# Optimization experiments

Measured on AMD Instinct MI355X. Metric: run time of the kernel, lower is better.

## Reference

```python
import jax, jax.numpy as jnp
import numpy as np

DAYS, TOPICS, T, E, H, DH = 30, 20, 128, 300, 256, 64

def _lstm_layer(x, Wih, Whh, b):
    # x: [B, T, D] -> (outputs [B, T, H], final hidden [B, H]); torch gate order i,f,g,o
    B = x.shape[0]
    Hh = Whh.shape[1]
    def step(carry, xt):
        h, c = carry
        g = xt @ Wih.T + h @ Whh.T + b
        i, f, gg, o = jnp.split(g, 4, axis=-1)
        c = jax.nn.sigmoid(f) * c + jax.nn.sigmoid(i) * jnp.tanh(gg)
        h = jax.nn.sigmoid(o) * jnp.tanh(c)
        return (h, c), h
    init = (jnp.zeros((B, Hh), x.dtype), jnp.zeros((B, Hh), x.dtype))
    (hT, _), ys = jax.lax.scan(step, init, jnp.swapaxes(x, 0, 1))
    return jnp.swapaxes(ys, 0, 1), hT

def _lstm2(x, W0, U0, b0, W1, U1, b1):
    # 2-layer LSTM (eval mode, dropout inactive). Returns layer-1 outputs and
    # LAYER-0 final hidden (the torch code indexes final_hidden_state[0]).
    y0, h0T = _lstm_layer(x, W0, U0, b0)
    y1, _ = _lstm_layer(y0, W1, U1, b1)
    return y1, h0T

def _attn_topic(out, final, w1_W, w1_b):
    # out [topics, H], final [H]; keep sorted weights until cumulative sum exceeds 0.8 (inclusive)
    score = (out @ w1_W.T + w1_b) @ final            # [topics]
    attn = jax.nn.softmax(score, axis=0)
    order = jnp.argsort(-attn)
    s = attn[order]
    keep = (jnp.cumsum(s) - s) <= 0.8                # exclusive-cumsum <= 0.8 == torch break-inclusive
    return jnp.sum((s * keep)[:, None] * out[order], axis=0)

def _forward(X, previous_labels,
             txt_Wih0, txt_Whh0, txt_b0, txt_Wih1, txt_Whh1, txt_b1,
             top_Wih0, top_Whh0, top_b0, top_Wih1, top_Whh1, top_b1,
             day_Wih0, day_Whh0, day_b0, day_Wih1, day_Whh1, day_b1,
             w1_W, w1_b, w2_W, w2_b, lin1_W, lin1_b, lin2_W, lin2_b,
             head_W, head_b):
    days, ntop, tlen, emb = X.shape
    # batch all (day, topic) sequences through the text LSTM at once
    x = X.reshape(days * ntop, tlen, emb)
    _, h_text = _lstm2(x, txt_Wih0, txt_Whh0, txt_b0, txt_Wih1, txt_Whh1, txt_b1)  # [days*ntop, H]
    topic_in = h_text.reshape(days, ntop, -1)
    y_top, h_top = _lstm2(topic_in, top_Wih0, top_Whh0, top_b0, top_Wih1, top_Whh1, top_b1)
    day_hidden = jax.vmap(lambda o, f: _attn_topic(o, f, w1_W, w1_b))(y_top, h_top)  # [days, H]
    y_day, h_day = _lstm2(day_hidden[None], day_Wih0, day_Whh0, day_b0, day_Wih1, day_Whh1, day_b1)
    score = (y_day[0] @ w2_W.T + w2_b) @ h_day[0]    # [days]
    attn = jax.nn.softmax(score, axis=0)
    ctx = attn @ y_day[0]                            # [64]
    h = ctx @ lin1_W.T + lin1_b
    h = h @ lin2_W.T + lin2_b                        # [16]
    feats = jnp.concatenate([jnp.broadcast_to(h, (4, h.shape[0])), previous_labels], axis=1)  # [4, 20]
    out = jnp.sum(feats * head_W, axis=1) + head_b   # [4] = (PCEDG, CCI, Retails, CPI)
    return out[:, None]                              # [4, 1]

def setup_inputs() -> dict:
    key = jax.random.key(0)
    ks = jax.random.split(key, 32)
    def p(i, shape, s=0.05):
        return (jax.random.normal(ks[i], shape) * s).astype(jnp.float32)
    return {
        "X": p(0, (DAYS, TOPICS, T, E), 1.0),
        "previous_labels": p(1, (4, 4), 1.0),
        "txt_Wih0": p(2, (4 * H, E)), "txt_Whh0": p(3, (4 * H, H)), "txt_b0": p(4, (4 * H,)),
        "txt_Wih1": p(5, (4 * H, H)), "txt_Whh1": p(6, (4 * H, H)), "txt_b1": p(7, (4 * H,)),
        "top_Wih0": p(8, (4 * H, H)), "top_Whh0": p(9, (4 * H, H)), "top_b0": p(10, (4 * H,)),
        "top_Wih1": p(11, (4 * H, H)), "top_Whh1": p(12, (4 * H, H)), "top_b1": p(13, (4 * H,)),
        "day_Wih0": p(14, (4 * DH, H)), "day_Whh0": p(15, (4 * DH, DH)), "day_b0": p(16, (4 * DH,)),
        "day_Wih1": p(17, (4 * DH, DH)), "day_Whh1": p(18, (4 * DH, DH)), "day_b1": p(19, (4 * DH,)),
        "w1_W": p(20, (H, H)), "w1_b": p(21, (H,)),
        "w2_W": p(22, (DH, DH)), "w2_b": p(23, (DH,)),
        "lin1_W": p(24, (48, DH)), "lin1_b": p(25, (48,)),
        "lin2_W": p(26, (16, 48)), "lin2_b": p(27, (16,)),
        "head_W": p(28, (4, 20)), "head_b": p(29, (4,)),
        "topics": TOPICS,
    }

def reference(X, previous_labels,
              txt_Wih0, txt_Whh0, txt_b0, txt_Wih1, txt_Whh1, txt_b1,
              top_Wih0, top_Whh0, top_b0, top_Wih1, top_Whh1, top_b1,
              day_Wih0, day_Whh0, day_b0, day_Wih1, day_Whh1, day_b1,
              w1_W, w1_b, w2_W, w2_b, lin1_W, lin1_b, lin2_W, lin2_b,
              head_W, head_b, topics):
    return _forward(X, previous_labels,
                    txt_Wih0, txt_Whh0, txt_b0, txt_Wih1, txt_Whh1, txt_b1,
                    top_Wih0, top_Whh0, top_b0, top_Wih1, top_Whh1, top_b1,
                    day_Wih0, day_Whh0, day_b0, day_Wih1, day_Whh1, day_b1,
                    w1_W, w1_b, w2_W, w2_b, lin1_W, lin1_b, lin2_W, lin2_b,
                    head_W, head_b)
```

## Files before the change

kernel.cpp:

```cpp
#include <hip/hip_runtime.h>
#include <hip/hip_bf16.h>


typedef __attribute__((ext_vector_type(8))) short short8;
typedef __attribute__((ext_vector_type(8))) __bf16 bf16x8;
typedef __attribute__((ext_vector_type(4))) float f4;

static __device__ __forceinline__ short f2bf(float f){
  unsigned u = __builtin_bit_cast(unsigned, f);
  u = u + 0x7fffu + ((u >> 16) & 1u);
  return (short)(u >> 16);
}
static __device__ __forceinline__ float b2f(short s){
  unsigned u = ((unsigned)(unsigned short)s) << 16;
  return __builtin_bit_cast(float, u);
}
static __device__ __forceinline__ float sigm(float x){ return 1.f/(1.f + __expf(-x)); }
static __device__ __forceinline__ float tanh_f(float x){
  float e = __expf(-2.f*fabsf(x));
  float t = (1.f - e)/(1.f + e);
  return x < 0.f ? -t : t;
}
static __device__ __forceinline__ f4 mfma16(short8 a, short8 b, f4 c){
  return __builtin_amdgcn_mfma_f32_16x16x32_bf16(
      __builtin_bit_cast(bf16x8, a), __builtin_bit_cast(bf16x8, b), c, 0, 0, 0);
}

__global__ void k_cvt_pad(const float* __restrict__ in, short* __restrict__ out,
                          int N, int K, int Kp){
  long total = (long)N * Kp;
  for (long i = (long)blockIdx.x*blockDim.x + threadIdx.x; i < total;
       i += (long)gridDim.x*blockDim.x){
    int k = (int)(i % Kp); long n = i / Kp;
    float v = (k < K) ? in[n*K + k] : 0.f;
    out[i] = f2bf(v);
  }
}

template<bool A_F32>
__global__ __launch_bounds__(256) void k_gemm(
    const void* __restrict__ Av, const short* __restrict__ Bt,
    const float* __restrict__ bias, short* __restrict__ C,
    int M, int N, int Kp, int Ka)
{
  int w = threadIdx.x >> 6, l = threadIdx.x & 63;
  int m0 = blockIdx.x*128 + w*32;
  int n0 = blockIdx.y*128;
  int lr = l & 15, lg = l >> 4;
  f4 acc[2][8];
  #pragma unroll
  for (int i=0;i<2;++i)
    #pragma unroll
    for (int j=0;j<8;++j) acc[i][j] = (f4){0.f,0.f,0.f,0.f};
  const float* Af = (const float*)Av;
  const short* Ab = (const short*)Av;
  int nkt = Kp >> 5;
  for (int kt = 0; kt < nkt; ++kt){
    int kb = kt*32 + lg*8;
    short8 a[2];
    #pragma unroll
    for (int mt = 0; mt < 2; ++mt){
      int m = m0 + mt*16 + lr;
      short8 av = {0,0,0,0,0,0,0,0};
      if (m < M){
        if (A_F32){
          if (kb + 7 < Ka){
            const float4* p4 = (const float4*)(Af + (long)m*Ka + kb);
            float4 x0 = p4[0], x1 = p4[1];
            av[0]=f2bf(x0.x); av[1]=f2bf(x0.y); av[2]=f2bf(x0.z); av[3]=f2bf(x0.w);
            av[4]=f2bf(x1.x); av[5]=f2bf(x1.y); av[6]=f2bf(x1.z); av[7]=f2bf(x1.w);
          } else {
            const float* p = Af + (long)m*Ka;
            #pragma unroll
            for (int j=0;j<8;++j) av[j] = (kb+j < Ka) ? f2bf(p[kb+j]) : (short)0;
          }
        } else {
          av = *(const short8*)(Ab + (long)m*Kp + kb);
        }
      }
      a[mt] = av;
    }
    #pragma unroll
    for (int nt = 0; nt < 8; ++nt){
      short8 b = *(const short8*)(Bt + (long)(n0 + nt*16 + lr)*Kp + kb);
      acc[0][nt] = mfma16(a[0], b, acc[0][nt]);
      acc[1][nt] = mfma16(a[1], b, acc[1][nt]);
    }
  }
  #pragma unroll
  for (int nt = 0; nt < 8; ++nt){
    int col = n0 + nt*16 + lr;
    float bv = bias ? bias[col] : 0.f;
    #pragma unroll
    for (int mt = 0; mt < 2; ++mt){
      #pragma unroll
      for (int r = 0; r < 4; ++r){
        int row = m0 + mt*16 + lg*4 + r;
        if (row < M) C[(long)row*N + col] = f2bf(acc[mt][nt][r] + bv);
      }
    }
  }
}

__global__ __launch_bounds__(256) void k_lstm_step(
    const short* __restrict__ G,
    const short* __restrict__ Whh,
    short* __restrict__ h_bf,
    float* __restrict__ c,
    short* __restrict__ y_bf,
    float* __restrict__ y_f32,
    float* __restrict__ h_f32,
    int nseq, int T, int t)
{
  __shared__ float gbuf[4*32*36];
  int w = threadIdx.x >> 6, l = threadIdx.x & 63;
  int s0 = blockIdx.x * 32;
  int u0 = blockIdx.y * 32;
  int lr = l & 15, lg = l >> 4;
  f4 acc[2][2];
  #pragma unroll
  for (int i=0;i<2;++i){ acc[i][0]=(f4){0,0,0,0}; acc[i][1]=(f4){0,0,0,0}; }
  if (t > 0){
    for (int kt = 0; kt < 8; ++kt){
      int kb = kt*32 + lg*8;
      short8 a[2];
      #pragma unroll
      for (int mt=0; mt<2; ++mt){
        int s = s0 + mt*16 + lr;
        short8 av = {0,0,0,0,0,0,0,0};
        if (s < nseq) av = *(const short8*)(h_bf + (long)s*256 + kb);
        a[mt] = av;
      }
      #pragma unroll
      for (int ntl=0; ntl<2; ++ntl){
        int row = w*256 + u0 + ntl*16 + lr;
        short8 b = *(const short8*)(Whh + (long)row*256 + kb);
        acc[0][ntl] = mfma16(a[0], b, acc[0][ntl]);
        acc[1][ntl] = mfma16(a[1], b, acc[1][ntl]);
      }
    }
  }
  #pragma unroll
  for (int ntl=0; ntl<2; ++ntl){
    int ur = ntl*16 + lr;
    int coln = w*256 + u0 + ur;
    #pragma unroll
    for (int mt=0; mt<2; ++mt){
      #pragma unroll
      for (int r=0;r<4;++r){
        int m = mt*16 + lg*4 + r;
        int s = s0 + m;
        float gv = acc[mt][ntl][r];
        if (s < nseq) gv += b2f(G[(long)(s*T + t)*1024 + coln]);
        gbuf[(w*32 + m)*36 + ur] = gv;
      }
    }
  }
  __syncthreads();
  for (int i = 0; i < 4; ++i){
    int idx = i*256 + threadIdx.x;
    int m = idx >> 5, ur = idx & 31;
    int s = s0 + m, u = u0 + ur;
    if (s >= nseq) continue;
    float gi = gbuf[(0*32+m)*36+ur];
    float gf = gbuf[(1*32+m)*36+ur];
    float gg = gbuf[(2*32+m)*36+ur];
    float go = gbuf[(3*32+m)*36+ur];
    float cold = (t>0) ? c[(long)s*256+u] : 0.f;
    float cn = sigm(gf)*cold + sigm(gi)*tanh_f(gg);
    float hn = sigm(go)*tanh_f(cn);
    c[(long)s*256+u] = cn;
    short hb = f2bf(hn);
    h_bf[(long)s*256+u] = hb;
    if (y_bf)  y_bf[(long)(s*T+t)*256 + u] = hb;
    if (y_f32) y_f32[(long)(s*T+t)*256 + u] = hn;
    if (h_f32) h_f32[(long)s*256+u] = hn;
  }
}

__global__ __launch_bounds__(1024) void k_day_lstm(
    const short* __restrict__ Gd,
    const float* __restrict__ Whh,
    short* __restrict__ y_bf,
    float* __restrict__ y_f32,
    float* __restrict__ hT_f32,
    int T)
{
  __shared__ float whhT[64*257];
  __shared__ float h[64], cc[64], part[4][256], gates[256];
  int tid = threadIdx.x;
  for (int i = tid; i < 256*64; i += 1024){
    int n = i >> 6, k = i & 63;
    whhT[k*257 + n] = Whh[i];
  }
  if (tid < 64){ h[tid]=0.f; cc[tid]=0.f; }
  __syncthreads();
  int n = tid & 255, kg = tid >> 8;
  for (int t = 0; t < T; ++t){
    float p = 0.f;
    #pragma unroll
    for (int kk = 0; kk < 16; ++kk){
      int k = kg*16 + kk;
      p += h[k]*whhT[k*257+n];
    }
    part[kg][n] = p;
    __syncthreads();
    if (tid < 256)
      gates[tid] = b2f(Gd[t*256+tid]) + part[0][tid]+part[1][tid]+part[2][tid]+part[3][tid];
    __syncthreads();
    if (tid < 64){
      float gi=gates[tid], gf=gates[64+tid], gg=gates[128+tid], go=gates[192+tid];
      float cn = sigm(gf)*cc[tid] + sigm(gi)*tanh_f(gg);
      float hn = sigm(go)*tanh_f(cn);
      cc[tid]=cn; h[tid]=hn;
      if (y_bf)  y_bf[t*64+tid]  = f2bf(hn);
      if (y_f32) y_f32[t*64+tid] = hn;
      if (hT_f32 && t==T-1) hT_f32[tid] = hn;
    }
    __syncthreads();
  }
}

__global__ __launch_bounds__(256) void k_topic_attn(
    const float* __restrict__ y1,
    const float* __restrict__ hT,
    const float* __restrict__ w1W, const float* __restrict__ w1b,
    short* __restrict__ dayh)
{
  int d = blockIdx.x, tid = threadIdx.x;
  __shared__ float hf[256], red[4], sc[20], wk[20], c0s;
  hf[tid] = hT[d*256+tid];
  __syncthreads();
  float v = 0.f;
  for (int j=0;j<256;++j) v += hf[j]*w1W[j*256+tid];
  float p0 = w1b[tid]*hf[tid];
  #pragma unroll
  for (int o=32;o>0;o>>=1) p0 += __shfl_down(p0,o);
  if ((tid&63)==0) red[tid>>6] = p0;
  __syncthreads();
  if (tid==0) c0s = red[0]+red[1]+red[2]+red[3];
  __syncthreads();
  for (int t=0;t<20;++t){
    float p = y1[(d*20+t)*256+tid]*v;
    #pragma unroll
    for (int o=32;o>0;o>>=1) p += __shfl_down(p,o);
    if ((tid&63)==0) red[tid>>6] = p;
    __syncthreads();
    if (tid==0) sc[t] = red[0]+red[1]+red[2]+red[3] + c0s;
    __syncthreads();
  }
  if (tid==0){
    float mx = -1e30f;
    for (int t=0;t<20;++t) mx = fmaxf(mx, sc[t]);
    float ss = 0.f;
    for (int t=0;t<20;++t){ sc[t] = __expf(sc[t]-mx); ss += sc[t]; }
    float inv = 1.f/ss;
    for (int t=0;t<20;++t) sc[t] *= inv;
    for (int t=0;t<20;++t){
      float pref = 0.f;
      for (int q=0;q<20;++q)
        if (sc[q]>sc[t] || (sc[q]==sc[t] && q<t)) pref += sc[q];
      wk[t] = (pref <= 0.8f) ? sc[t] : 0.f;
    }
  }
  __syncthreads();
  float a = 0.f;
  for (int t=0;t<20;++t) a += wk[t]*y1[(d*20+t)*256+tid];
  dayh[d*256+tid] = f2bf(a);
}

__global__ __launch_bounds__(64) void k_final(
    const float* __restrict__ y1,
    const float* __restrict__ hT,
    const float* __restrict__ w2W, const float* __restrict__ w2b,
    const float* __restrict__ l1W, const float* __restrict__ l1b,
    const float* __restrict__ l2W, const float* __restrict__ l2b,
    const float* __restrict__ hW,  const float* __restrict__ hb,
    const float* __restrict__ prev, float* __restrict__ out)
{
  int tid = threadIdx.x;
  __shared__ float hf[64], v2[64], sc[30], ctx[64], h1[48], h2[16], c0s;
  hf[tid] = hT[tid];
  __syncthreads();
  { float v=0.f; for (int j=0;j<64;++j) v += hf[j]*w2W[j*64+tid]; v2[tid]=v; }
  if (tid==0){ float c0=0.f; for (int j=0;j<64;++j) c0 += w2b[j]*hf[j]; c0s=c0; }
  __syncthreads();
  if (tid<30){ float s=c0s; for (int k=0;k<64;++k) s += y1[tid*64+k]*v2[k]; sc[tid]=s; }
  __syncthreads();
  if (tid==0){
    float mx=-1e30f; for (int d=0;d<30;++d) mx=fmaxf(mx,sc[d]);
    float ss=0.f; for (int d=0;d<30;++d){ sc[d]=__expf(sc[d]-mx); ss+=sc[d]; }
    float inv=1.f/ss; for (int d=0;d<30;++d) sc[d]*=inv;
  }
  __syncthreads();
  { float cx=0.f; for (int d=0;d<30;++d) cx += sc[d]*y1[d*64+tid]; ctx[tid]=cx; }
  __syncthreads();
  if (tid<48){ float s=l1b[tid]; for (int k=0;k<64;++k) s += ctx[k]*l1W[tid*64+k]; h1[tid]=s; }
  __syncthreads();
  if (tid<16){ float s=l2b[tid]; for (int k=0;k<48;++k) s += h1[k]*l2W[tid*48+k]; h2[tid]=s; }
  __syncthreads();
  if (tid<4){
    float s = hb[tid];
    for (int cI=0;cI<16;++cI) s += h2[cI]*hW[tid*20+cI];
    for (int cI=0;cI<4; ++cI) s += prev[tid*4+cI]*hW[tid*20+16+cI];
    out[tid] = s;
  }
}

extern "C" void kernel_launch(void* const* d_in, const int* in_sizes, int n_in,
                              void* d_out, int out_size, void* d_ws, size_t ws_size,
                              hipStream_t stream)
{
  const float* X        = (const float*)d_in[0];
  const float* prev     = (const float*)d_in[1];
  const float* tWih0    = (const float*)d_in[2];
  const float* tWhh0    = (const float*)d_in[3];
  const float* tb0      = (const float*)d_in[4];
  const float* pWih0    = (const float*)d_in[8];
  const float* pWhh0    = (const float*)d_in[9];
  const float* pb0      = (const float*)d_in[10];
  const float* pWih1    = (const float*)d_in[11];
  const float* pWhh1    = (const float*)d_in[12];
  const float* pb1      = (const float*)d_in[13];
  const float* dWih0    = (const float*)d_in[14];
  const float* dWhh0    = (const float*)d_in[15];
  const float* db0      = (const float*)d_in[16];
  const float* dWih1    = (const float*)d_in[17];
  const float* dWhh1    = (const float*)d_in[18];
  const float* db1      = (const float*)d_in[19];
  const float* w1W      = (const float*)d_in[20];
  const float* w1b      = (const float*)d_in[21];
  const float* w2W      = (const float*)d_in[22];
  const float* w2b      = (const float*)d_in[23];
  const float* l1W      = (const float*)d_in[24];
  const float* l1b      = (const float*)d_in[25];
  const float* l2W      = (const float*)d_in[26];
  const float* l2b      = (const float*)d_in[27];
  const float* hW       = (const float*)d_in[28];
  const float* hb       = (const float*)d_in[29];
  float* out = (float*)d_out;

  char* wsb = (char*)d_ws;
  size_t off = 0;
  auto alloc = [&](size_t bytes)->void*{
    void* p = wsb + off;
    off = (off + bytes + 255) & ~(size_t)255;
    return p;
  };
  short* G0      = (short*)alloc((size_t)76800*1024*2);
  short* WihT    = (short*)alloc((size_t)1024*320*2);
  short* Whh0b   = (short*)alloc((size_t)1024*256*2);
  short* pW0i    = (short*)alloc((size_t)1024*256*2);
  short* pW0h    = (short*)alloc((size_t)1024*256*2);
  short* pW1i    = (short*)alloc((size_t)1024*256*2);
  short* pW1h    = (short*)alloc((size_t)1024*256*2);
  short* dW0i    = (short*)alloc((size_t)256*256*2);
  short* dW1i    = (short*)alloc((size_t)256*64*2);
  short* h_text  = (short*)alloc((size_t)600*256*2);
  float* c_text  = (float*)alloc((size_t)600*256*4);
  short* Gt0     = (short*)alloc((size_t)600*1024*2);
  short* h_t0    = (short*)alloc((size_t)30*256*2);
  float* c_t0    = (float*)alloc((size_t)30*256*4);
  short* y_t0    = (short*)alloc((size_t)600*256*2);
  float* h_topf  = (float*)alloc((size_t)30*256*4);
  short* Gt1     = (short*)alloc((size_t)600*1024*2);
  short* h_t1    = (short*)alloc((size_t)30*256*2);
  float* c_t1    = (float*)alloc((size_t)30*256*4);
  float* y_t1f   = (float*)alloc((size_t)600*256*4);
  short* dayh    = (short*)alloc((size_t)30*256*2);
  short* Gd0     = (short*)alloc((size_t)30*256*2);
  short* y_d0    = (short*)alloc((size_t)30*64*2);
  float* h_d0f   = (float*)alloc((size_t)64*4);
  short* Gd1     = (short*)alloc((size_t)30*256*2);
  float* y_d1f   = (float*)alloc((size_t)30*64*4);
  (void)ws_size; (void)in_sizes; (void)n_in; (void)out_size;

  k_cvt_pad<<<512,256,0,stream>>>(tWih0, WihT, 1024, 300, 320);
  k_cvt_pad<<<512,256,0,stream>>>(tWhh0, Whh0b, 1024, 256, 256);
  k_cvt_pad<<<512,256,0,stream>>>(pWih0, pW0i, 1024, 256, 256);
  k_cvt_pad<<<512,256,0,stream>>>(pWhh0, pW0h, 1024, 256, 256);
  k_cvt_pad<<<512,256,0,stream>>>(pWih1, pW1i, 1024, 256, 256);
  k_cvt_pad<<<512,256,0,stream>>>(pWhh1, pW1h, 1024, 256, 256);
  k_cvt_pad<<<256,256,0,stream>>>(dWih0, dW0i, 256, 256, 256);
  k_cvt_pad<<<64,256,0,stream>>>(dWih1, dW1i, 256, 64, 64);

  k_gemm<true><<<dim3(600,8),256,0,stream>>>((const void*)X, WihT, tb0, G0,
                                             76800, 1024, 320, 300);
  for (int t = 0; t < 128; ++t)
    k_lstm_step<<<dim3(19,8),256,0,stream>>>(G0, Whh0b, h_text, c_text,
                                             nullptr, nullptr, nullptr, 600, 128, t);
  k_gemm<false><<<dim3(5,8),256,0,stream>>>((const void*)h_text, pW0i, pb0, Gt0,
                                            600, 1024, 256, 256);
  for (int t = 0; t < 20; ++t)
    k_lstm_step<<<dim3(1,8),256,0,stream>>>(Gt0, pW0h, h_t0, c_t0,
                                            y_t0, nullptr, h_topf, 30, 20, t);
  k_gemm<false><<<dim3(5,8),256,0,stream>>>((const void*)y_t0, pW1i, pb1, Gt1,
                                            600, 1024, 256, 256);
  for (int t = 0; t < 20; ++t)
    k_lstm_step<<<dim3(1,8),256,0,stream>>>(Gt1, pW1h, h_t1, c_t1,
                                            nullptr, y_t1f, nullptr, 30, 20, t);
  k_topic_attn<<<30,256,0,stream>>>(y_t1f, h_topf, w1W, w1b, dayh);
  k_gemm<false><<<dim3(1,2),256,0,stream>>>((const void*)dayh, dW0i, db0, Gd0,
                                            30, 256, 256, 256);
  k_day_lstm<<<1,1024,0,stream>>>(Gd0, dWhh0, y_d0, nullptr, h_d0f, 30);
  k_gemm<false><<<dim3(1,2),256,0,stream>>>((const void*)y_d0, dW1i, db1, Gd1,
                                            30, 256, 64, 64);
  k_day_lstm<<<1,1024,0,stream>>>(Gd1, dWhh1, nullptr, y_d1f, nullptr, 30);
  k_final<<<1,64,0,stream>>>(y_d1f, h_d0f, w2W, w2b, l1W, l1b, l2W, l2b,
                             hW, hb, prev, out);
}
```

Baseline: 2.405 ms.

## Run each LSTM layer as one persistent kernel with MFMA-fragment weight layout

Replaces the per-timestep LSTM launches (128 + 20 + 20 launches) with a single persistent kernel per layer. Each block keeps its 32 sequences' hidden state in LDS as MFMA fragments and its cell state in registers across all timesteps. Weights are pre-repacked into MFMA-fragment order, the input GEMM gets a new kernel that stages A in LDS and registers, and gate outputs are written time-major so the recurrent kernel reads them contiguously. The cost is far less parallelism: the text LSTM runs on only 19 blocks and each topic layer on 1 block, each streaming all of Whh from global/L2 every step.

Result: slower. 3.957 ms (+64.5%).

```diff
diff --git a/kernel.cpp b/kernel.cpp
--- a/kernel.cpp
+++ b/kernel.cpp
@@ -37,8 +37,214 @@
   }
 }
 
+__global__ void k_cvt_repack(const float* __restrict__ in, short* __restrict__ out,
+                             int N, int K, int KT){
+  long total = (long)(N/16) * KT * 64;
+  for (long idx = (long)blockIdx.x*blockDim.x + threadIdx.x; idx < total;
+       idx += (long)gridDim.x*blockDim.x){
+    int l  = (int)(idx & 63);
+    long f = idx >> 6;
+    int kt = (int)(f % KT);
+    int nt = (int)(f / KT);
+    int row = nt*16 + (l & 15);
+    int kb  = kt*32 + (l >> 4)*8;
+    #pragma unroll
+    for (int e = 0; e < 8; ++e){
+      int k = kb + e;
+      float v = (k < K) ? in[(long)row*K + k] : 0.f;
+      out[idx*8 + e] = f2bf(v);
+    }
+  }
+}
+
+template<bool A_F32, int KT>
+__global__ __launch_bounds__(256, 2) void k_gemm_big(
+    const void* __restrict__ Av, const short* __restrict__ W4,
+    const float* __restrict__ bias, short* __restrict__ Cout,
+    int M, int Ka, int TT, int SS)
+{
+  constexpr int Kp = KT*32;
+  __shared__ short Afr[4*KT*64*8];
+  __shared__ short Cst[64*128];
+  int tid = threadIdx.x;
+  int w = tid >> 6, l = tid & 63, lr = l & 15, lg = l >> 4;
+  int m0 = blockIdx.x*64;
+  const float* Af = (const float*)Av;
+  const short* Ab = (const short*)Av;
+
+  for (int i2 = tid; i2 < 64*(Kp/8); i2 += 256){
+    int row = i2 / (Kp/8);
+    int kb  = (i2 % (Kp/8))*8;
+    int mt = row >> 4, kt = kb >> 5, ls = (row & 15) + 16*((kb & 31) >> 3);
+    short8 v = {0,0,0,0,0,0,0,0};
+    int grow = m0 + row;
+    if (grow < M){
+      if (A_F32){
+        #pragma unroll
+        for (int e = 0; e < 8; ++e){
+          int k = kb + e;
+          v[e] = (k < Ka) ? f2bf(Af[(long)grow*Ka + k]) : (short)0;
+        }
+      } else {
+        v = *(const short8*)(Ab + (long)grow*Kp + kb);
+      }
+    }
+    *(short8*)&Afr[(((mt*KT) + kt)*64 + ls)*8] = v;
+  }
+  __syncthreads();
+
+  short8 areg[4][KT];
+  #pragma unroll
+  for (int mt = 0; mt < 4; ++mt)
+    #pragma unroll
+    for (int kt = 0; kt < KT; ++kt)
+      areg[mt][kt] = *(const short8*)&Afr[(((mt*KT) + kt)*64 + l)*8];
+
+  for (int nc = 0; nc < 8; ++nc){
+    f4 acc[4][2];
+    #pragma unroll
+    for (int mt = 0; mt < 4; ++mt){ acc[mt][0]=(f4){0,0,0,0}; acc[mt][1]=(f4){0,0,0,0}; }
+    #pragma unroll
+    for (int kt = 0; kt < KT; ++kt){
+      short8 b0 = *(const short8*)&W4[(((long)(nc*8 + w*2 + 0)*KT + kt)*64 + l)*8];
+      short8 b1 = *(const short8*)&W4[(((long)(nc*8 + w*2 + 1)*KT + kt)*64 + l)*8];
+      #pragma unroll
+      for (int mt = 0; mt < 4; ++mt){
+        acc[mt][0] = mfma16(areg[mt][kt], b0, acc[mt][0]);
+        acc[mt][1] = mfma16(areg[mt][kt], b1, acc[mt][1]);
+      }
+    }
+    __syncthreads();
+    #pragma unroll
+    for (int jj = 0; jj < 2; ++jj){
+      int cl = w*32 + jj*16 + lr;
+      float bv = bias ? bias[nc*128 + cl] : 0.f;
+      #pragma unroll
+      for (int mt = 0; mt < 4; ++mt){
+        #pragma unroll
+        for (int r = 0; r < 4; ++r)
+          Cst[(mt*16 + lg*4 + r)*128 + cl] = f2bf(acc[mt][jj][r] + bv);
+      }
+    }
+    __syncthreads();
+    #pragma unroll
+    for (int it = 0; it < 4; ++it){
+      int row = it*16 + (tid >> 4);
+      int grow = m0 + row;
+      if (grow < M){
+        long prow = (long)(grow % TT)*SS + grow/TT;
+        *(short8*)(Cout + prow*1024 + nc*128 + (tid & 15)*8) =
+            *(const short8*)&Cst[row*128 + (tid & 15)*8];
+      }
+    }
+  }
+}
+
+__global__ __launch_bounds__(512, 2) void k_lstm_seq(
+    const short* __restrict__ G, const short* __restrict__ W4h,
+    short* __restrict__ y_bf,
+    float* __restrict__ y_f32,
+    short* __restrict__ hfin_bf,
+    float* __restrict__ hfin_f32,
+    int NS, int T)
+{
+  __shared__ short hfrag[2*8*64*8];
+  __shared__ short gx[1024*32];
+  int tid = threadIdx.x;
+  int w = tid >> 6, l = tid & 63, lr = l & 15, lg = l >> 4;
+  int s  = tid & 31;
+  int ub = (tid >> 5) * 16;
+  int s0 = blockIdx.x * 32;
+  int ns = NS - s0; if (ns > 32) ns = 32;
+
+  for (int i = tid; i < 2*8*64*8; i += 512) hfrag[i] = 0;
+  float c[16];
+  #pragma unroll
+  for (int i = 0; i < 16; ++i) c[i] = 0.f;
+  __syncthreads();
+
+  for (int t = 0; t < T; ++t){
+    short8 ga[4], gb[4];
+    if (s < ns){
+      const short* gp = G + ((long)t*NS + s0 + s)*1024 + ub;
+      #pragma unroll
+      for (int g = 0; g < 4; ++g){
+        ga[g] = *(const short8*)(gp + g*256);
+        gb[g] = *(const short8*)(gp + g*256 + 8);
+      }
+    } else {
+      #pragma unroll
+      for (int g = 0; g < 4; ++g){ ga[g] = (short8){0,0,0,0,0,0,0,0}; gb[g] = ga[g]; }
+    }
+    f4 acc[2][8];
+    #pragma unroll
+    for (int j = 0; j < 8; ++j){ acc[0][j]=(f4){0,0,0,0}; acc[1][j]=(f4){0,0,0,0}; }
+    #pragma unroll
+    for (int kt = 0; kt < 8; ++kt){
+      short8 a0 = *(const short8*)&hfrag[((0*8 + kt)*64 + l)*8];
+      short8 a1 = *(const short8*)&hfrag[((1*8 + kt)*64 + l)*8];
+      #pragma unroll
+      for (int j = 0; j < 8; ++j){
+        short8 b = *(const short8*)&W4h[((((w*8 + j)*8) + kt)*64 + l)*8];
+        acc[0][j] = mfma16(a0, b, acc[0][j]);
+        acc[1][j] = mfma16(a1, b, acc[1][j]);
+      }
+    }
+    #pragma unroll
+    for (int j = 0; j < 8; ++j){
+      int col = w*128 + j*16 + lr;
+      #pragma unroll
+      for (int mt = 0; mt < 2; ++mt){
+        ushort4 v;
+        v.x = (unsigned short)f2bf(acc[mt][j][0]);
+        v.y = (unsigned short)f2bf(acc[mt][j][1]);
+        v.z = (unsigned short)f2bf(acc[mt][j][2]);
+        v.w = (unsigned short)f2bf(acc[mt][j][3]);
+        *(ushort4*)&gx[col*32 + mt*16 + lg*4] = v;
+      }
+    }
+    __syncthreads();
+    if (s < ns){
+      short8 hv0, hv1;
+      #pragma unroll
+      for (int i = 0; i < 16; ++i){
+        int u = ub + i;
+        short gsi = (i < 8) ? ga[0][i & 7] : gb[0][i & 7];
+        short gsf = (i < 8) ? ga[1][i & 7] : gb[1][i & 7];
+        short gsg = (i < 8) ? ga[2][i & 7] : gb[2][i & 7];
+        short gso = (i < 8) ? ga[3][i & 7] : gb[3][i & 7];
+        float gi = b2f(gsi) + b2f(gx[(0*256 + u)*32 + s]);
+        float gf = b2f(gsf) + b2f(gx[(1*256 + u)*32 + s]);
+        float gg = b2f(gsg) + b2f(gx[(2*256 + u)*32 + s]);
+        float go = b2f(gso) + b2f(gx[(3*256 + u)*32 + s]);
+        float cn = sigm(gf)*c[i] + sigm(gi)*tanh_f(gg);
+        float hn = sigm(go)*tanh_f(cn);
+        c[i] = cn;
+        short hb = f2bf(hn);
+        if (i < 8) hv0[i & 7] = hb; else hv1[i & 7] = hb;
+        if (y_f32) y_f32[((long)t*NS + s0 + s)*256 + u] = hn;
+        if (hfin_f32 && t == T-1) hfin_f32[(long)(s0 + s)*256 + u] = hn;
+      }
+      int mt = s >> 4, kt = ub >> 5;
+      int l1 = (s & 15) + 16*((ub & 31) >> 3);
+      int l2 = (s & 15) + 16*(((ub + 8) & 31) >> 3);
+      *(short8*)&hfrag[((mt*8 + kt)*64 + l1)*8] = hv0;
+      *(short8*)&hfrag[((mt*8 + kt)*64 + l2)*8] = hv1;
+      if (y_bf){
+        short* yp = y_bf + ((long)t*NS + s0 + s)*256 + ub;
+        *(short8*)yp = hv0; *(short8*)(yp + 8) = hv1;
+      }
+      if (hfin_bf && t == T-1){
+        short* hp = hfin_bf + (long)(s0 + s)*256 + ub;
+        *(short8*)hp = hv0; *(short8*)(hp + 8) = hv1;
+      }
+    }
+    __syncthreads();
+  }
+}
+
 template<bool A_F32>
-__global__ __launch_bounds__(256) void k_gemm(
+__global__ __launch_bounds__(256) void k_gemm_flat(
     const void* __restrict__ Av, const short* __restrict__ Bt,
     const float* __restrict__ bias, short* __restrict__ C,
     int M, int N, int Kp, int Ka)
@@ -52,7 +258,6 @@
   for (int i=0;i<2;++i)
     #pragma unroll
     for (int j=0;j<8;++j) acc[i][j] = (f4){0.f,0.f,0.f,0.f};
-  const float* Af = (const float*)Av;
   const short* Ab = (const short*)Av;
   int nkt = Kp >> 5;
   for (int kt = 0; kt < nkt; ++kt){
@@ -62,22 +267,7 @@
     for (int mt = 0; mt < 2; ++mt){
       int m = m0 + mt*16 + lr;
       short8 av = {0,0,0,0,0,0,0,0};
-      if (m < M){
-        if (A_F32){
-          if (kb + 7 < Ka){
-            const float4* p4 = (const float4*)(Af + (long)m*Ka + kb);
-            float4 x0 = p4[0], x1 = p4[1];
-            av[0]=f2bf(x0.x); av[1]=f2bf(x0.y); av[2]=f2bf(x0.z); av[3]=f2bf(x0.w);
-            av[4]=f2bf(x1.x); av[5]=f2bf(x1.y); av[6]=f2bf(x1.z); av[7]=f2bf(x1.w);
-          } else {
-            const float* p = Af + (long)m*Ka;
-            #pragma unroll
-            for (int j=0;j<8;++j) av[j] = (kb+j < Ka) ? f2bf(p[kb+j]) : (short)0;
-          }
-        } else {
-          av = *(const short8*)(Ab + (long)m*Kp + kb);
-        }
-      }
+      if (m < M) av = *(const short8*)(Ab + (long)m*Kp + kb);
       a[mt] = av;
     }
     #pragma unroll
@@ -99,82 +289,6 @@
         if (row < M) C[(long)row*N + col] = f2bf(acc[mt][nt][r] + bv);
       }
     }
-  }
-}
-
-__global__ __launch_bounds__(256) void k_lstm_step(
-    const short* __restrict__ G,
-    const short* __restrict__ Whh,
-    short* __restrict__ h_bf,
-    float* __restrict__ c,
-    short* __restrict__ y_bf,
-    float* __restrict__ y_f32,
-    float* __restrict__ h_f32,
-    int nseq, int T, int t)
-{
-  __shared__ float gbuf[4*32*36];
-  int w = threadIdx.x >> 6, l = threadIdx.x & 63;
-  int s0 = blockIdx.x * 32;
-  int u0 = blockIdx.y * 32;
-  int lr = l & 15, lg = l >> 4;
-  f4 acc[2][2];
-  #pragma unroll
-  for (int i=0;i<2;++i){ acc[i][0]=(f4){0,0,0,0}; acc[i][1]=(f4){0,0,0,0}; }
-  if (t > 0){
-    for (int kt = 0; kt < 8; ++kt){
-      int kb = kt*32 + lg*8;
-      short8 a[2];
-      #pragma unroll
-      for (int mt=0; mt<2; ++mt){
-        int s = s0 + mt*16 + lr;
-        short8 av = {0,0,0,0,0,0,0,0};
-        if (s < nseq) av = *(const short8*)(h_bf + (long)s*256 + kb);
-        a[mt] = av;
-      }
-      #pragma unroll
-      for (int ntl=0; ntl<2; ++ntl){
-        int row = w*256 + u0 + ntl*16 + lr;
-        short8 b = *(const short8*)(Whh + (long)row*256 + kb);
-        acc[0][ntl] = mfma16(a[0], b, acc[0][ntl]);
-        acc[1][ntl] = mfma16(a[1], b, acc[1][ntl]);
-      }
-    }
-  }
-  #pragma unroll
-  for (int ntl=0; ntl<2; ++ntl){
-    int ur = ntl*16 + lr;
-    int coln = w*256 + u0 + ur;
-    #pragma unroll
-    for (int mt=0; mt<2; ++mt){
-      #pragma unroll
-      for (int r=0;r<4;++r){
-        int m = mt*16 + lg*4 + r;
-        int s = s0 + m;
-        float gv = acc[mt][ntl][r];
-        if (s < nseq) gv += b2f(G[(long)(s*T + t)*1024 + coln]);
-        gbuf[(w*32 + m)*36 + ur] = gv;
-      }
-    }
-  }
-  __syncthreads();
-  for (int i = 0; i < 4; ++i){
-    int idx = i*256 + threadIdx.x;
-    int m = idx >> 5, ur = idx & 31;
-    int s = s0 + m, u = u0 + ur;
-    if (s >= nseq) continue;
-    float gi = gbuf[(0*32+m)*36+ur];
-    float gf = gbuf[(1*32+m)*36+ur];
-    float gg = gbuf[(2*32+m)*36+ur];
-    float go = gbuf[(3*32+m)*36+ur];
-    float cold = (t>0) ? c[(long)s*256+u] : 0.f;
-    float cn = sigm(gf)*cold + sigm(gi)*tanh_f(gg);
-    float hn = sigm(go)*tanh_f(cn);
-    c[(long)s*256+u] = cn;
-    short hb = f2bf(hn);
-    h_bf[(long)s*256+u] = hb;
-    if (y_bf)  y_bf[(long)(s*T+t)*256 + u] = hb;
-    if (y_f32) y_f32[(long)(s*T+t)*256 + u] = hn;
-    if (h_f32) h_f32[(long)s*256+u] = hn;
   }
 }
 
@@ -222,8 +336,7 @@
 }
 
 __global__ __launch_bounds__(256) void k_topic_attn(
-    const float* __restrict__ y1,
-    const float* __restrict__ hT,
+    const float* __restrict__ y1, const float* __restrict__ hT,
     const float* __restrict__ w1W, const float* __restrict__ w1b,
     short* __restrict__ dayh)
 {
@@ -241,7 +354,7 @@
   if (tid==0) c0s = red[0]+red[1]+red[2]+red[3];
   __syncthreads();
   for (int t=0;t<20;++t){
-    float p = y1[(d*20+t)*256+tid]*v;
+    float p = y1[(t*30 + d)*256 + tid]*v;
     #pragma unroll
     for (int o=32;o>0;o>>=1) p += __shfl_down(p,o);
     if ((tid&63)==0) red[tid>>6] = p;
@@ -265,13 +378,12 @@
   }
   __syncthreads();
   float a = 0.f;
-  for (int t=0;t<20;++t) a += wk[t]*y1[(d*20+t)*256+tid];
+  for (int t=0;t<20;++t) a += wk[t]*y1[(t*30 + d)*256 + tid];
   dayh[d*256+tid] = f2bf(a);
 }
 
 __global__ __launch_bounds__(64) void k_final(
-    const float* __restrict__ y1,
-    const float* __restrict__ hT,
+    const float* __restrict__ y1,  const float* __restrict__ hT,
     const float* __restrict__ w2W, const float* __restrict__ w2b,
     const float* __restrict__ l1W, const float* __restrict__ l1b,
     const float* __restrict__ l2W, const float* __restrict__ l2b,
@@ -285,7 +397,7 @@
   { float v=0.f; for (int j=0;j<64;++j) v += hf[j]*w2W[j*64+tid]; v2[tid]=v; }
   if (tid==0){ float c0=0.f; for (int j=0;j<64;++j) c0 += w2b[j]*hf[j]; c0s=c0; }
   __syncthreads();
-  if (tid<30){ float s=c0s; for (int k=0;k<64;++k) s += y1[tid*64+k]*v2[k]; sc[tid]=s; }
+  if (tid<30){ float sacc=c0s; for (int k=0;k<64;++k) sacc += y1[tid*64+k]*v2[k]; sc[tid]=sacc; }
   __syncthreads();
   if (tid==0){
     float mx=-1e30f; for (int d=0;d<30;++d) mx=fmaxf(mx,sc[d]);
@@ -295,15 +407,15 @@
   __syncthreads();
   { float cx=0.f; for (int d=0;d<30;++d) cx += sc[d]*y1[d*64+tid]; ctx[tid]=cx; }
   __syncthreads();
-  if (tid<48){ float s=l1b[tid]; for (int k=0;k<64;++k) s += ctx[k]*l1W[tid*64+k]; h1[tid]=s; }
-  __syncthreads();
-  if (tid<16){ float s=l2b[tid]; for (int k=0;k<48;++k) s += h1[k]*l2W[tid*48+k]; h2[tid]=s; }
+  if (tid<48){ float sacc=l1b[tid]; for (int k=0;k<64;++k) sacc += ctx[k]*l1W[tid*64+k]; h1[tid]=sacc; }
+  __syncthreads();
+  if (tid<16){ float sacc=l2b[tid]; for (int k=0;k<48;++k) sacc += h1[k]*l2W[tid*48+k]; h2[tid]=sacc; }
   __syncthreads();
   if (tid<4){
-    float s = hb[tid];
-    for (int cI=0;cI<16;++cI) s += h2[cI]*hW[tid*20+cI];
-    for (int cI=0;cI<4; ++cI) s += prev[tid*4+cI]*hW[tid*20+16+cI];
-    out[tid] = s;
+    float sacc = hb[tid];
+    for (int cI=0;cI<16;++cI) sacc += h2[cI]*hW[tid*20+cI];
+    for (int cI=0;cI<4; ++cI) sacc += prev[tid*4+cI]*hW[tid*20+16+cI];
+    out[tid] = sacc;
   }
 }
 
@@ -347,26 +459,21 @@
     off = (off + bytes + 255) & ~(size_t)255;
     return p;
   };
-  short* G0      = (short*)alloc((size_t)76800*1024*2);
-  short* WihT    = (short*)alloc((size_t)1024*320*2);
-  short* Whh0b   = (short*)alloc((size_t)1024*256*2);
-  short* pW0i    = (short*)alloc((size_t)1024*256*2);
-  short* pW0h    = (short*)alloc((size_t)1024*256*2);
-  short* pW1i    = (short*)alloc((size_t)1024*256*2);
-  short* pW1h    = (short*)alloc((size_t)1024*256*2);
+  short* G0      = (short*)alloc((size_t)128*600*1024*2);
+  short* W4tWih  = (short*)alloc((size_t)1024*320*2);
+  short* W4tWhh  = (short*)alloc((size_t)1024*256*2);
+  short* W4p0i   = (short*)alloc((size_t)1024*256*2);
+  short* W4p0h   = (short*)alloc((size_t)1024*256*2);
+  short* W4p1i   = (short*)alloc((size_t)1024*256*2);
+  short* W4p1h   = (short*)alloc((size_t)1024*256*2);
   short* dW0i    = (short*)alloc((size_t)256*256*2);
   short* dW1i    = (short*)alloc((size_t)256*64*2);
   short* h_text  = (short*)alloc((size_t)600*256*2);
-  float* c_text  = (float*)alloc((size_t)600*256*4);
-  short* Gt0     = (short*)alloc((size_t)600*1024*2);
-  short* h_t0    = (short*)alloc((size_t)30*256*2);
-  float* c_t0    = (float*)alloc((size_t)30*256*4);
-  short* y_t0    = (short*)alloc((size_t)600*256*2);
+  short* Gt0     = (short*)alloc((size_t)20*30*1024*2);
+  short* y_t0    = (short*)alloc((size_t)20*30*256*2);
   float* h_topf  = (float*)alloc((size_t)30*256*4);
-  short* Gt1     = (short*)alloc((size_t)600*1024*2);
-  short* h_t1    = (short*)alloc((size_t)30*256*2);
-  float* c_t1    = (float*)alloc((size_t)30*256*4);
-  float* y_t1f   = (float*)alloc((size_t)600*256*4);
+  short* Gt1     = (short*)alloc((size_t)20*30*1024*2);
+  float* y_t1f   = (float*)alloc((size_t)20*30*256*4);
   short* dayh    = (short*)alloc((size_t)30*256*2);
   short* Gd0     = (short*)alloc((size_t)30*256*2);
   short* y_d0    = (short*)alloc((size_t)30*64*2);
@@ -375,36 +482,33 @@
   float* y_d1f   = (float*)alloc((size_t)30*64*4);
   (void)ws_size; (void)in_sizes; (void)n_in; (void)out_size;
 
-  k_cvt_pad<<<512,256,0,stream>>>(tWih0, WihT, 1024, 300, 320);
-  k_cvt_pad<<<512,256,0,stream>>>(tWhh0, Whh0b, 1024, 256, 256);
-  k_cvt_pad<<<512,256,0,stream>>>(pWih0, pW0i, 1024, 256, 256);
-  k_cvt_pad<<<512,256,0,stream>>>(pWhh0, pW0h, 1024, 256, 256);
-  k_cvt_pad<<<512,256,0,stream>>>(pWih1, pW1i, 1024, 256, 256);
-  k_cvt_pad<<<512,256,0,stream>>>(pWhh1, pW1h, 1024, 256, 256);
+  k_cvt_repack<<<256,256,0,stream>>>(tWih0, W4tWih, 1024, 300, 10);
+  k_cvt_repack<<<256,256,0,stream>>>(tWhh0, W4tWhh, 1024, 256, 8);
+  k_cvt_repack<<<256,256,0,stream>>>(pWih0, W4p0i, 1024, 256, 8);
+  k_cvt_repack<<<256,256,0,stream>>>(pWhh0, W4p0h, 1024, 256, 8);
+  k_cvt_repack<<<256,256,0,stream>>>(pWih1, W4p1i, 1024, 256, 8);
+  k_cvt_repack<<<256,256,0,stream>>>(pWhh1, W4p1h, 1024, 256, 8);
   k_cvt_pad<<<256,256,0,stream>>>(dWih0, dW0i, 256, 256, 256);
   k_cvt_pad<<<64,256,0,stream>>>(dWih1, dW1i, 256, 64, 64);
 
-  k_gemm<true><<<dim3(600,8),256,0,stream>>>((const void*)X, WihT, tb0, G0,
-                                             76800, 1024, 320, 300);
-  for (int t = 0; t < 128; ++t)
-    k_lstm_step<<<dim3(19,8),256,0,stream>>>(G0, Whh0b, h_text, c_text,
-                                             nullptr, nullptr, nullptr, 600, 128, t);
-  k_gemm<false><<<dim3(5,8),256,0,stream>>>((const void*)h_text, pW0i, pb0, Gt0,
-                                            600, 1024, 256, 256);
-  for (int t = 0; t < 20; ++t)
-    k_lstm_step<<<dim3(1,8),256,0,stream>>>(Gt0, pW0h, h_t0, c_t0,
-                                            y_t0, nullptr, h_topf, 30, 20, t);
-  k_gemm<false><<<dim3(5,8),256,0,stream>>>((const void*)y_t0, pW1i, pb1, Gt1,
-                                            600, 1024, 256, 256);
-  for (int t = 0; t < 20; ++t)
-    k_lstm_step<<<dim3(1,8),256,0,stream>>>(Gt1, pW1h, h_t1, c_t1,
-                                            nullptr, y_t1f, nullptr, 30, 20, t);
+  k_gemm_big<true,10><<<1200,256,0,stream>>>((const void*)X, W4tWih, tb0, G0,
+                                             76800, 300, 128, 600);
+  k_lstm_seq<<<19,512,0,stream>>>(G0, W4tWhh, nullptr, nullptr,
+                                  h_text, nullptr, 600, 128);
+  k_gemm_big<false,8><<<10,256,0,stream>>>((const void*)h_text, W4p0i, pb0, Gt0,
+                                           600, 256, 20, 30);
+  k_lstm_seq<<<1,512,0,stream>>>(Gt0, W4p0h, y_t0, nullptr,
+                                 nullptr, h_topf, 30, 20);
+  k_gemm_big<false,8><<<10,256,0,stream>>>((const void*)y_t0, W4p1i, pb1, Gt1,
+                                           600, 256, 1, 600);
+  k_lstm_seq<<<1,512,0,stream>>>(Gt1, W4p1h, nullptr, y_t1f,
+                                 nullptr, nullptr, 30, 20);
   k_topic_attn<<<30,256,0,stream>>>(y_t1f, h_topf, w1W, w1b, dayh);
-  k_gemm<false><<<dim3(1,2),256,0,stream>>>((const void*)dayh, dW0i, db0, Gd0,
-                                            30, 256, 256, 256);
+  k_gemm_flat<false><<<dim3(1,2),256,0,stream>>>((const void*)dayh, dW0i, db0, Gd0,
+                                                 30, 256, 256, 256);
   k_day_lstm<<<1,1024,0,stream>>>(Gd0, dWhh0, y_d0, nullptr, h_d0f, 30);
-  k_gemm<false><<<dim3(1,2),256,0,stream>>>((const void*)y_d0, dW1i, db1, Gd1,
-                                            30, 256, 64, 64);
+  k_gemm_flat<false><<<dim3(1,2),256,0,stream>>>((const void*)y_d0, dW1i, db1, Gd1,
+                                                 30, 256, 64, 64);
   k_day_lstm<<<1,1024,0,stream>>>(Gd1, dWhh1, nullptr, y_d1f, nullptr, 30);
   k_final<<<1,64,0,stream>>>(y_d1f, h_d0f, w2W, w2b, l1W, l1b, l2W, l2b,
                              hW, hb, prev, out);
```
